# Kernel tuning notes

Measured on AMD Instinct MI355X. Metric: run time of the kernel, lower is better.

## Reference

```python
import jax, jax.numpy as jnp
import numpy as np

D_MODEL = 1024
NUM_HEADS = 16
D_K = D_MODEL // NUM_HEADS
B, S = 2, 2048


def setup_inputs() -> dict:
    key = jax.random.key(0)
    ks = jax.random.split(key, 11)
    scale = 1.0 / np.sqrt(D_MODEL)
    inp = {
        "q": jax.random.normal(ks[0], (B, S, D_MODEL), dtype=jnp.float32),
        "k": jax.random.normal(ks[1], (B, S, D_MODEL), dtype=jnp.float32),
        "v": jax.random.normal(ks[2], (B, S, D_MODEL), dtype=jnp.float32),
        "w_q": jax.random.normal(ks[3], (D_MODEL, D_MODEL), dtype=jnp.float32) * scale,
        "b_q": jnp.zeros((D_MODEL,), dtype=jnp.float32),
        "w_k": jax.random.normal(ks[4], (D_MODEL, D_MODEL), dtype=jnp.float32) * scale,
        "b_k": jnp.zeros((D_MODEL,), dtype=jnp.float32),
        "w_v": jax.random.normal(ks[5], (D_MODEL, D_MODEL), dtype=jnp.float32) * scale,
        "b_v": jnp.zeros((D_MODEL,), dtype=jnp.float32),
        "w_o": jax.random.normal(ks[6], (D_MODEL, D_MODEL), dtype=jnp.float32) * scale,
        "b_o": jnp.zeros((D_MODEL,), dtype=jnp.float32),
    }
    return inp


def reference(q, k, v, w_q, b_q, w_k, b_k, w_v, b_v, w_o, b_o):
    # Linear projections (torch Linear: x @ W^T + b)
    def proj(x, w, b):
        # [B,S,D] -> [B,H,S,d_k]
        y = x @ w.T + b
        return y.reshape(B, S, NUM_HEADS, D_K).transpose(0, 2, 1, 3)

    query = proj(q, w_q, b_q)
    key_ = proj(k, w_k, b_k)
    value = proj(v, w_v, b_v)

    # scores: [B,H,S,S]
    scores = jnp.einsum('bhqd,bhkd->bhqk', query, key_) / jnp.sqrt(
        jnp.asarray(D_K, dtype=query.dtype))
    attn = jax.nn.softmax(scores, axis=-1)
    x = jnp.einsum('bhqk,bhkd->bhqd', attn, value)
    x = x.transpose(0, 2, 1, 3).reshape(B, S, D_MODEL)
    return x @ w_o.T + b_o
```

## Files before the change

### kernel.cpp

```cpp
#include <hip/hip_runtime.h>
#include <stdint.h>

#define D_MODEL 1024
#define NHEAD 16
#define DK 64
#define BATCH 2
#define SEQ 2048
#define MROWS (BATCH * SEQ)
#define KVB 64
#define NIT (SEQ / KVB)
#define QSCALE 0.18033688011112042f

typedef __attribute__((ext_vector_type(8))) __bf16 bf16x8;
typedef __attribute__((ext_vector_type(2))) __bf16 bf16x2;
typedef __attribute__((ext_vector_type(4))) float f32x4;
typedef __attribute__((ext_vector_type(4))) unsigned int u32x4;
typedef __attribute__((ext_vector_type(2))) unsigned int u32x2;

#if defined(__has_builtin)
#if __has_builtin(__builtin_amdgcn_permlane32_swap) && \
    __has_builtin(__builtin_amdgcn_permlane16_swap)
#define HAVE_PERMLANE_SWAP 1
#endif
#endif
#ifndef HAVE_PERMLANE_SWAP
#define HAVE_PERMLANE_SWAP 0
#endif

__device__ __forceinline__ float exp2_hw(float x) {
  return __builtin_amdgcn_exp2f(x);
}

__device__ __forceinline__ f32x4 f4zero() {
  f32x4 z = {0.f, 0.f, 0.f, 0.f};
  return z;
}

__device__ __forceinline__ f32x4 mfma_bf16(bf16x8 a, bf16x8 b, f32x4 c) {
  return __builtin_amdgcn_mfma_f32_16x16x32_bf16(a, b, c, 0, 0, 0);
}

__device__ __forceinline__ void gload_lds16(const void* g, void* l) {
  __builtin_amdgcn_global_load_lds(
      (const __attribute__((address_space(1))) unsigned int*)g,
      (__attribute__((address_space(3))) unsigned int*)l, 16, 0, 0);
}

__device__ __forceinline__ unsigned short f2b(float x) {
  unsigned int u = __float_as_uint(x);
  u += 0x7fffu + ((u >> 16) & 1u);
  return (unsigned short)(u >> 16);
}

#if HAVE_PERMLANE_SWAP
__device__ __forceinline__ u32x2 pl32(unsigned int a, unsigned int b) {
  return __builtin_amdgcn_permlane32_swap(a, b, false, false);
}
__device__ __forceinline__ u32x2 pl16(unsigned int a, unsigned int b) {
  return __builtin_amdgcn_permlane16_swap(a, b, false, false);
}
#endif

__global__ void cvt_all_kernel(const float* __restrict__ q, const float* __restrict__ k,
                               const float* __restrict__ v, const float* __restrict__ wq,
                               const float* __restrict__ wk, const float* __restrict__ wv,
                               const float* __restrict__ wo,
                               unsigned short* __restrict__ actout,
                               unsigned short* __restrict__ wout) {
  const size_t SZA = (size_t)MROWS * D_MODEL;
  const size_t SZW = (size_t)D_MODEL * D_MODEL;
  const int bid = blockIdx.x;
  const float* in;
  unsigned short* out;
  int i;
  if (bid < 12288) {
    const int seg = bid >> 12, ib = bid & 4095;
    in = seg == 0 ? q : seg == 1 ? k : v;
    out = actout + (size_t)seg * SZA;
    i = ib * 256 + threadIdx.x;
  } else {
    const int b2 = bid - 12288;
    const int seg = b2 >> 10, ib = b2 & 1023;
    in = seg == 0 ? wq : seg == 1 ? wk : seg == 2 ? wv : wo;
    out = wout + (size_t)seg * SZW;
    i = ib * 256 + threadIdx.x;
  }
  float4 x = ((const float4*)in)[i];
  ushort4 r;
  r.x = f2b(x.x); r.y = f2b(x.y); r.z = f2b(x.z); r.w = f2b(x.w);
  ((ushort4*)out)[i] = r;
}

template <int EPI, int BROW>
__device__ __forceinline__ void gemm_body128(const unsigned short* __restrict__ A,
                                             const unsigned short* __restrict__ B,
                                             const float* __restrict__ bias,
                                             float scale,
                                             unsigned short* __restrict__ outb,
                                             float* __restrict__ outf, int bx,
                                             int M, int N, int K,
                                             unsigned short* sA, unsigned short* sB) {
  const int tid = threadIdx.x;
  const int w = tid >> 6, l = tid & 63;
  const int nTN = N >> 7;
  const int bm = bx / nTN, bn = bx % nTN;
  const int rowBase = bm << 7, colBase = bn << 7;
  const int wm = w >> 1, wn = w & 1;
  const int g = l >> 4, c16 = l & 15;

  f32x4 acc[4][4];
#pragma unroll
  for (int i = 0; i < 4; i++)
#pragma unroll
    for (int j = 0; j < 4; j++) acc[i][j] = f4zero();

  const int rloc = l >> 2;
  const int uch = (l & 3) ^ (rloc & 3);

  for (int kk = 0; kk < K; kk += 32) {
    __syncthreads();
#pragma unroll
    for (int h = 0; h < 2; h++) {
      const int r0 = w * 16 + h * 64;
      gload_lds16(A + (size_t)(rowBase + r0 + rloc) * K + kk + uch * 8,
                  &sA[r0 * 32]);
      gload_lds16(B + (size_t)(colBase + r0 + rloc) * K + kk + uch * 8,
                  &sB[r0 * 32]);
    }
    __syncthreads();

    bf16x8 af[4], bfr[4];
#pragma unroll
    for (int mt = 0; mt < 4; mt++) {
      const int r = wm * 64 + mt * 16 + c16;
      af[mt] = *(const bf16x8*)&sA[r * 32 + (g ^ (r & 3)) * 8];
    }
#pragma unroll
    for (int nt = 0; nt < 4; nt++) {
      const int r = wn * 64 + nt * 16 + c16;
      bfr[nt] = *(const bf16x8*)&sB[r * 32 + (g ^ (r & 3)) * 8];
    }
#pragma unroll
    for (int mt = 0; mt < 4; mt++)
#pragma unroll
      for (int nt = 0; nt < 4; nt++)
        acc[mt][nt] = mfma_bf16(af[mt], bfr[nt], acc[mt][nt]);
  }

#pragma unroll
  for (int mt = 0; mt < 4; mt++) {
    float brow[4];
    if (BROW) {
#pragma unroll
      for (int i = 0; i < 4; i++)
        brow[i] = bias[rowBase + wm * 64 + mt * 16 + g * 4 + i];
    }
#pragma unroll
    for (int nt = 0; nt < 4; nt++) {
      const int col = colBase + wn * 64 + nt * 16 + c16;
      const float bcol = BROW ? 0.f : bias[col];
#pragma unroll
      for (int i = 0; i < 4; i++) {
        const int row = rowBase + wm * 64 + mt * 16 + g * 4 + i;
        const float bv = BROW ? brow[i] : bcol;
        const float v = (acc[mt][nt][i] + bv) * scale;
        if (EPI == 0)
          outb[(size_t)row * N + col] = f2b(v);
        else
          outf[(size_t)row * N + col] = v;
      }
    }
  }
}

__device__ __forceinline__ void gemm_body64(const unsigned short* __restrict__ A,
                                            const unsigned short* __restrict__ B,
                                            const float* __restrict__ bias,
                                            float* __restrict__ outf, int bx,
                                            int M, int N, int K,
                                            unsigned short* sA, unsigned short* sB) {
  const int tid = threadIdx.x;
  const int w = tid >> 6, l = tid & 63;
  const int nTN = N >> 6;
  const int bm = bx / nTN, bn = bx % nTN;
  const int rowBase = bm << 7, colBase = bn << 6;
  const int g = l >> 4, c16 = l & 15;

  f32x4 acc[2][4];
#pragma unroll
  for (int i = 0; i < 2; i++)
#pragma unroll
    for (int j = 0; j < 4; j++) acc[i][j] = f4zero();

  const int rloc = l >> 2;
  const int uch = (l & 3) ^ (rloc & 3);

  for (int kk = 0; kk < K; kk += 32) {
    __syncthreads();
    gload_lds16(A + (size_t)(rowBase + w * 16 + rloc) * K + kk + uch * 8,
                &sA[(w * 16) * 32]);
    gload_lds16(A + (size_t)(rowBase + 64 + w * 16 + rloc) * K + kk + uch * 8,
                &sA[(64 + w * 16) * 32]);
    gload_lds16(B + (size_t)(colBase + w * 16 + rloc) * K + kk + uch * 8,
                &sB[(w * 16) * 32]);
    __syncthreads();

    bf16x8 af[2], bfr[4];
#pragma unroll
    for (int mt = 0; mt < 2; mt++) {
      const int r = w * 32 + mt * 16 + c16;
      af[mt] = *(const bf16x8*)&sA[r * 32 + (g ^ (r & 3)) * 8];
    }
#pragma unroll
    for (int nt = 0; nt < 4; nt++) {
      const int r = nt * 16 + c16;
      bfr[nt] = *(const bf16x8*)&sB[r * 32 + (g ^ (r & 3)) * 8];
    }
#pragma unroll
    for (int mt = 0; mt < 2; mt++)
#pragma unroll
      for (int nt = 0; nt < 4; nt++)
        acc[mt][nt] = mfma_bf16(af[mt], bfr[nt], acc[mt][nt]);
  }

#pragma unroll
  for (int mt = 0; mt < 2; mt++)
#pragma unroll
    for (int nt = 0; nt < 4; nt++) {
      const int col = colBase + nt * 16 + c16;
      const float bv = bias[col];
#pragma unroll
      for (int i = 0; i < 4; i++) {
        const int row = rowBase + w * 32 + mt * 16 + g * 4 + i;
        outf[(size_t)row * N + col] = acc[mt][nt][i] + bv;
      }
    }
}

__global__ __launch_bounds__(256, 2) void gemm_qkv_kernel(
    const unsigned short* __restrict__ Abase, const unsigned short* __restrict__ Wbase,
    const float* __restrict__ bq, const float* __restrict__ bk,
    const float* __restrict__ bv, unsigned short* __restrict__ QKout,
    unsigned short* __restrict__ VTout) {
  __shared__ __attribute__((aligned(16))) unsigned short sA[128 * 32];
  __shared__ __attribute__((aligned(16))) unsigned short sB[128 * 32];
  const int nblk = 256;
  const int gid = blockIdx.x / nblk, bx = blockIdx.x % nblk;
  const size_t SZA = (size_t)MROWS * D_MODEL;
  const size_t SZW = (size_t)D_MODEL * D_MODEL;
  if (gid < 2) {
    const float* bias = gid == 0 ? bq : bk;
    const float scale = gid == 0 ? QSCALE : 1.0f;
    gemm_body128<0, 0>(Abase + (size_t)gid * SZA, Wbase + (size_t)gid * SZW, bias,
                       scale, QKout + (size_t)gid * SZA, nullptr, bx, MROWS,
                       D_MODEL, D_MODEL, sA, sB);
  } else {
    gemm_body128<0, 1>(Wbase + 2 * SZW, Abase + 2 * SZA, bv, 1.0f, VTout, nullptr,
                       bx, D_MODEL, MROWS, D_MODEL, sA, sB);
  }
}

__global__ __launch_bounds__(256, 4) void gemm_out_kernel(
    const unsigned short* __restrict__ A, const unsigned short* __restrict__ B,
    const float* __restrict__ bias, float* __restrict__ out) {
  __shared__ __attribute__((aligned(16))) unsigned short sA[128 * 32];
  __shared__ __attribute__((aligned(16))) unsigned short sB[64 * 32];
  gemm_body64(A, B, bias, out, blockIdx.x, MROWS, D_MODEL, D_MODEL, sA, sB);
}

__global__ __launch_bounds__(256, 2) void attn_kernel(
    const unsigned short* __restrict__ Qh, const unsigned short* __restrict__ Kh,
    const unsigned short* __restrict__ Vt, unsigned short* __restrict__ Xh) {
  __shared__ __attribute__((aligned(16))) unsigned short sK[2][KVB * 64];
  __shared__ __attribute__((aligned(16))) unsigned short sV[2][64 * KVB];

  const int tid = threadIdx.x, w = tid >> 6, l = tid & 63;
  const int fid = blockIdx.x;
  const int L = (fid & 7) * 64 + (fid >> 3);
  const int bh = L >> 4, qx = L & 15;
  const int b = bh >> 4, h = bh & 15;
  const int q0 = qx * 128 + w * 32;
  const int g = l >> 4, c16 = l & 15;

  bf16x8 qf[2][2];
#pragma unroll
  for (int qs = 0; qs < 2; ++qs)
#pragma unroll
    for (int f = 0; f < 2; ++f)
      qf[qs][f] = *(const bf16x8*)&Qh[(size_t)(b * SEQ + q0 + qs * 16 + c16) * D_MODEL +
                                      h * DK + f * 32 + g * 8];

  const u32x4 onesu = {0x3F803F80u, 0x3F803F80u, 0x3F803F80u, 0x3F803F80u};
  const bf16x8 onesf = __builtin_bit_cast(bf16x8, onesu);

  f32x4 acc[2][4], accl[2];
#pragma unroll
  for (int qs = 0; qs < 2; ++qs) {
#pragma unroll
    for (int dt = 0; dt < 4; ++dt) acc[qs][dt] = f4zero();
    accl[qs] = f4zero();
  }

  const int srow = l >> 3, sch = (l & 7) ^ (srow & 7);

  auto STAGE = [&](int pbuf, int kv0) {
#pragma unroll
    for (int hh = 0; hh < 2; ++hh) {
      const int r0 = w * 16 + hh * 8;
      gload_lds16(
          Kh + (size_t)(b * SEQ + kv0 + r0 + srow) * D_MODEL + h * DK + sch * 8,
          &sK[pbuf][r0 * 64]);
      gload_lds16(Vt + (size_t)(h * DK + r0 + srow) * MROWS + b * SEQ + kv0 + sch * 8,
                  &sV[pbuf][r0 * 64]);
    }
  };

  auto STEP = [&](int PB) {
    f32x4 st[2][4];
#pragma unroll
    for (int kt = 0; kt < 4; ++kt) {
      bf16x8 kf[2];
#pragma unroll
      for (int f = 0; f < 2; ++f) {
        const int key = kt * 16 + c16;
        const int ch = (f * 4 + g) ^ (key & 7);
        kf[f] = *(const bf16x8*)&sK[PB][key * 64 + ch * 8];
      }
#pragma unroll
      for (int qs = 0; qs < 2; ++qs) {
        f32x4 s = mfma_bf16(kf[0], qf[qs][0], f4zero());
        st[qs][kt] = mfma_bf16(kf[1], qf[qs][1], s);
      }
    }

    unsigned int Qpk[2][4][2];
#pragma unroll
    for (int qs = 0; qs < 2; ++qs)
#pragma unroll
      for (int kt = 0; kt < 4; ++kt) {
        float pv[4];
#pragma unroll
        for (int i = 0; i < 4; ++i) pv[i] = exp2_hw(st[qs][kt][i]);
#pragma unroll
        for (int hh = 0; hh < 2; ++hh) {
          bf16x2 t2;
          t2.x = (__bf16)pv[hh * 2];
          t2.y = (__bf16)pv[hh * 2 + 1];
          Qpk[qs][kt][hh] = __builtin_bit_cast(unsigned int, t2);
        }
      }

#pragma unroll
    for (int ks = 0; ks < 2; ++ks) {
      bf16x8 pfrag[2];
#pragma unroll
      for (int qs = 0; qs < 2; ++qs) {
        unsigned int pw[4];
#if HAVE_PERMLANE_SWAP
#pragma unroll
        for (int hh = 0; hh < 2; ++hh) {
          u32x2 s1 = pl32(Qpk[qs][2 * ks][hh], Qpk[qs][2 * ks + 1][hh]);
          u32x2 s2 = pl16(s1.x, s1.y);
          pw[hh] = s2.x;
          pw[2 + hh] = s2.y;
        }
#else
#pragma unroll
        for (int hh = 0; hh < 2; ++hh) {
          const unsigned int a = Qpk[qs][2 * ks][hh], bb = Qpk[qs][2 * ks + 1][hh];
          const unsigned int as = __shfl_xor((int)a, 32);
          const unsigned int bs = __shfl_xor((int)bb, 32);
          const unsigned int r0 = (l >= 32) ? bs : a;
          const unsigned int r1 = (l >= 32) ? bb : as;
          const unsigned int t0 = __shfl_xor((int)r0, 16);
          const unsigned int t1 = __shfl_xor((int)r1, 16);
          pw[hh] = (g & 1) ? t1 : r0;
          pw[2 + hh] = (g & 1) ? r1 : t0;
        }
#endif
        u32x4 pv4 = {pw[0], pw[1], pw[2], pw[3]};
        pfrag[qs] = __builtin_bit_cast(bf16x8, pv4);
      }
      accl[0] = mfma_bf16(pfrag[0], onesf, accl[0]);
      accl[1] = mfma_bf16(pfrag[1], onesf, accl[1]);
#pragma unroll
      for (int dt = 0; dt < 4; ++dt) {
        const int d = dt * 16 + c16;
        const int ch = (ks * 4 + g) ^ (d & 7);
        bf16x8 vfrag = *(const bf16x8*)&sV[PB][d * 64 + ch * 8];
        acc[0][dt] = mfma_bf16(pfrag[0], vfrag, acc[0][dt]);
        acc[1][dt] = mfma_bf16(pfrag[1], vfrag, acc[1][dt]);
      }
    }
  };

  STAGE(0, 0);
  __syncthreads();

  for (int it = 0; it < NIT; it += 2) {
    if (it + 1 < NIT) STAGE(1, (it + 1) * KVB);
    STEP(0);
    __syncthreads();
    if (it + 2 < NIT) STAGE(0, (it + 2) * KVB);
    STEP(1);
    __syncthreads();
  }

#pragma unroll
  for (int qs = 0; qs < 2; ++qs) {
    float linv[4];
#pragma unroll
    for (int i = 0; i < 4; ++i) linv[i] = __builtin_amdgcn_rcpf(accl[qs][i]);
#pragma unroll
    for (int dt = 0; dt < 4; ++dt)
#pragma unroll
      for (int i = 0; i < 4; ++i) {
        const int row = b * SEQ + q0 + qs * 16 + g * 4 + i;
        const int col = h * DK + dt * 16 + c16;
        Xh[(size_t)row * D_MODEL + col] = f2b(acc[qs][dt][i] * linv[i]);
      }
  }
}

extern "C" void kernel_launch(void* const* d_in, const int* in_sizes, int n_in,
                              void* d_out, int out_size, void* d_ws, size_t ws_size,
                              hipStream_t stream) {
  (void)in_sizes; (void)n_in; (void)out_size; (void)ws_size;
  const float* q = (const float*)d_in[0];
  const float* k = (const float*)d_in[1];
  const float* v = (const float*)d_in[2];
  const float* w_q = (const float*)d_in[3];
  const float* b_q = (const float*)d_in[4];
  const float* w_k = (const float*)d_in[5];
  const float* b_k = (const float*)d_in[6];
  const float* w_v = (const float*)d_in[7];
  const float* b_v = (const float*)d_in[8];
  const float* w_o = (const float*)d_in[9];
  const float* b_o = (const float*)d_in[10];

  const size_t SZ_ACT = (size_t)MROWS * D_MODEL;
  const size_t SZ_W = (size_t)D_MODEL * D_MODEL;
  char* ws = (char*)d_ws;
  unsigned short* qb = (unsigned short*)(ws);
  unsigned short* Xh = (unsigned short*)(ws);
  unsigned short* Qproj = (unsigned short*)(ws + 6 * SZ_ACT);
  unsigned short* Vt = (unsigned short*)(ws + 10 * SZ_ACT);
  unsigned short* wqb = (unsigned short*)(ws + 12 * SZ_ACT);
  unsigned short* wob = (unsigned short*)(ws + 12 * SZ_ACT + 6 * SZ_W);

  cvt_all_kernel<<<16384, 256, 0, stream>>>(q, k, v, w_q, w_k, w_v, w_o, qb, wqb);

  gemm_qkv_kernel<<<3 * 256, 256, 0, stream>>>(qb, wqb, b_q, b_k, b_v, Qproj, Vt);

  attn_kernel<<<512, 256, 0, stream>>>(Qproj, Qproj + SZ_ACT, Vt, Xh);

  gemm_out_kernel<<<512, 256, 0, stream>>>(Xh, wob, b_o, (float*)d_out);
}
```

Before: 118.6 us.

## Double attention KV tile to 128 keys, add setprio around PV MFMAs

```diff
diff --git a/kernel.cpp b/kernel.cpp
--- a/kernel.cpp
+++ b/kernel.cpp
@@ -7,7 +7,7 @@
 #define BATCH 2
 #define SEQ 2048
 #define MROWS (BATCH * SEQ)
-#define KVB 64
+#define KVB 128
 #define NIT (SEQ / KVB)
 #define QSCALE 0.18033688011112042f
 
@@ -237,7 +237,7 @@
     }
 }
 
-__global__ __launch_bounds__(256, 2) void gemm_qkv_kernel(
+__global__ __launch_bounds__(256, 3) void gemm_qkv_kernel(
     const unsigned short* __restrict__ Abase, const unsigned short* __restrict__ Wbase,
     const float* __restrict__ bq, const float* __restrict__ bk,
     const float* __restrict__ bv, unsigned short* __restrict__ QKout,
@@ -271,8 +271,8 @@
 __global__ __launch_bounds__(256, 2) void attn_kernel(
     const unsigned short* __restrict__ Qh, const unsigned short* __restrict__ Kh,
     const unsigned short* __restrict__ Vt, unsigned short* __restrict__ Xh) {
-  __shared__ __attribute__((aligned(16))) unsigned short sK[2][KVB * 64];
-  __shared__ __attribute__((aligned(16))) unsigned short sV[2][64 * KVB];
+  __shared__ __attribute__((aligned(16))) unsigned short sK[2][2][64 * 64];
+  __shared__ __attribute__((aligned(16))) unsigned short sV[2][2][64 * 64];
 
   const int tid = threadIdx.x, w = tid >> 6, l = tid & 63;
   const int fid = blockIdx.x;
@@ -305,17 +305,21 @@
 
   auto STAGE = [&](int pbuf, int kv0) {
 #pragma unroll
-    for (int hh = 0; hh < 2; ++hh) {
-      const int r0 = w * 16 + hh * 8;
-      gload_lds16(
-          Kh + (size_t)(b * SEQ + kv0 + r0 + srow) * D_MODEL + h * DK + sch * 8,
-          &sK[pbuf][r0 * 64]);
-      gload_lds16(Vt + (size_t)(h * DK + r0 + srow) * MROWS + b * SEQ + kv0 + sch * 8,
-                  &sV[pbuf][r0 * 64]);
-    }
+    for (int half = 0; half < 2; ++half)
+#pragma unroll
+      for (int hh = 0; hh < 2; ++hh) {
+        const int r0 = w * 16 + hh * 8;
+        const int kvh = kv0 + half * 64;
+        gload_lds16(
+            Kh + (size_t)(b * SEQ + kvh + r0 + srow) * D_MODEL + h * DK + sch * 8,
+            &sK[pbuf][half][r0 * 64]);
+        gload_lds16(
+            Vt + (size_t)(h * DK + r0 + srow) * MROWS + b * SEQ + kvh + sch * 8,
+            &sV[pbuf][half][r0 * 64]);
+      }
   };
 
-  auto STEP = [&](int PB) {
+  auto STEPH = [&](const unsigned short* sKp, const unsigned short* sVp) {
     f32x4 st[2][4];
 #pragma unroll
     for (int kt = 0; kt < 4; ++kt) {
@@ -324,7 +328,7 @@
       for (int f = 0; f < 2; ++f) {
         const int key = kt * 16 + c16;
         const int ch = (f * 4 + g) ^ (key & 7);
-        kf[f] = *(const bf16x8*)&sK[PB][key * 64 + ch * 8];
+        kf[f] = *(const bf16x8*)&sKp[key * 64 + ch * 8];
       }
 #pragma unroll
       for (int qs = 0; qs < 2; ++qs) {
@@ -381,16 +385,18 @@
         u32x4 pv4 = {pw[0], pw[1], pw[2], pw[3]};
         pfrag[qs] = __builtin_bit_cast(bf16x8, pv4);
       }
+      __builtin_amdgcn_s_setprio(1);
       accl[0] = mfma_bf16(pfrag[0], onesf, accl[0]);
       accl[1] = mfma_bf16(pfrag[1], onesf, accl[1]);
 #pragma unroll
       for (int dt = 0; dt < 4; ++dt) {
         const int d = dt * 16 + c16;
         const int ch = (ks * 4 + g) ^ (d & 7);
-        bf16x8 vfrag = *(const bf16x8*)&sV[PB][d * 64 + ch * 8];
+        bf16x8 vfrag = *(const bf16x8*)&sVp[d * 64 + ch * 8];
         acc[0][dt] = mfma_bf16(pfrag[0], vfrag, acc[0][dt]);
         acc[1][dt] = mfma_bf16(pfrag[1], vfrag, acc[1][dt]);
       }
+      __builtin_amdgcn_s_setprio(0);
     }
   };
 
@@ -399,10 +405,12 @@
 
   for (int it = 0; it < NIT; it += 2) {
     if (it + 1 < NIT) STAGE(1, (it + 1) * KVB);
-    STEP(0);
+    STEPH(&sK[0][0][0], &sV[0][0][0]);
+    STEPH(&sK[0][1][0], &sV[0][1][0]);
     __syncthreads();
     if (it + 2 < NIT) STAGE(0, (it + 2) * KVB);
-    STEP(1);
+    STEPH(&sK[1][0][0], &sV[1][0][0]);
+    STEPH(&sK[1][1][0], &sV[1][1][0]);
     __syncthreads();
   }
 
```

After: 117.1 us. Within noise of the previous version (-1.2%).

## Split attention KV range in two and add a combine kernel

Applied to the files above, without the earlier changes.

```diff
diff --git a/kernel.cpp b/kernel.cpp
--- a/kernel.cpp
+++ b/kernel.cpp
@@ -8,7 +8,7 @@
 #define SEQ 2048
 #define MROWS (BATCH * SEQ)
 #define KVB 64
-#define NIT (SEQ / KVB)
+#define NITS 16
 #define QSCALE 0.18033688011112042f
 
 typedef __attribute__((ext_vector_type(8))) __bf16 bf16x8;
@@ -50,6 +50,13 @@
   unsigned int u = __float_as_uint(x);
   u += 0x7fffu + ((u >> 16) & 1u);
   return (unsigned short)(u >> 16);
+}
+
+__device__ __forceinline__ unsigned short f2h(float x) {
+  return __builtin_bit_cast(unsigned short, (_Float16)x);
+}
+__device__ __forceinline__ float h2f(unsigned short u) {
+  return (float)__builtin_bit_cast(_Float16, u);
 }
 
 #if HAVE_PERMLANE_SWAP
@@ -237,7 +244,7 @@
     }
 }
 
-__global__ __launch_bounds__(256, 2) void gemm_qkv_kernel(
+__global__ __launch_bounds__(256, 3) void gemm_qkv_kernel(
     const unsigned short* __restrict__ Abase, const unsigned short* __restrict__ Wbase,
     const float* __restrict__ bq, const float* __restrict__ bk,
     const float* __restrict__ bv, unsigned short* __restrict__ QKout,
@@ -268,18 +275,21 @@
   gemm_body64(A, B, bias, out, blockIdx.x, MROWS, D_MODEL, D_MODEL, sA, sB);
 }
 
-__global__ __launch_bounds__(256, 2) void attn_kernel(
+__global__ __launch_bounds__(256, 4) void attn_kernel(
     const unsigned short* __restrict__ Qh, const unsigned short* __restrict__ Kh,
-    const unsigned short* __restrict__ Vt, unsigned short* __restrict__ Xh) {
+    const unsigned short* __restrict__ Vt, unsigned short* __restrict__ Opart,
+    float* __restrict__ denout) {
   __shared__ __attribute__((aligned(16))) unsigned short sK[2][KVB * 64];
   __shared__ __attribute__((aligned(16))) unsigned short sV[2][64 * KVB];
 
   const int tid = threadIdx.x, w = tid >> 6, l = tid & 63;
   const int fid = blockIdx.x;
-  const int L = (fid & 7) * 64 + (fid >> 3);
-  const int bh = L >> 4, qx = L & 15;
+  const int L = (fid & 7) * 128 + (fid >> 3);
+  const int bh = L >> 5, rem = L & 31;
+  const int split = rem >> 4, qx = rem & 15;
   const int b = bh >> 4, h = bh & 15;
   const int q0 = qx * 128 + w * 32;
+  const int kvbase = split * (SEQ / 2);
   const int g = l >> 4, c16 = l & 15;
 
   bf16x8 qf[2][2];
@@ -307,10 +317,11 @@
 #pragma unroll
     for (int hh = 0; hh < 2; ++hh) {
       const int r0 = w * 16 + hh * 8;
-      gload_lds16(
-          Kh + (size_t)(b * SEQ + kv0 + r0 + srow) * D_MODEL + h * DK + sch * 8,
-          &sK[pbuf][r0 * 64]);
-      gload_lds16(Vt + (size_t)(h * DK + r0 + srow) * MROWS + b * SEQ + kv0 + sch * 8,
+      gload_lds16(Kh + (size_t)(b * SEQ + kvbase + kv0 + r0 + srow) * D_MODEL +
+                      h * DK + sch * 8,
+                  &sK[pbuf][r0 * 64]);
+      gload_lds16(Vt + (size_t)(h * DK + r0 + srow) * MROWS + b * SEQ + kvbase +
+                      kv0 + sch * 8,
                   &sV[pbuf][r0 * 64]);
     }
   };
@@ -381,6 +392,7 @@
         u32x4 pv4 = {pw[0], pw[1], pw[2], pw[3]};
         pfrag[qs] = __builtin_bit_cast(bf16x8, pv4);
       }
+      __builtin_amdgcn_s_setprio(1);
       accl[0] = mfma_bf16(pfrag[0], onesf, accl[0]);
       accl[1] = mfma_bf16(pfrag[1], onesf, accl[1]);
 #pragma unroll
@@ -391,21 +403,24 @@
         acc[0][dt] = mfma_bf16(pfrag[0], vfrag, acc[0][dt]);
         acc[1][dt] = mfma_bf16(pfrag[1], vfrag, acc[1][dt]);
       }
+      __builtin_amdgcn_s_setprio(0);
     }
   };
 
   STAGE(0, 0);
   __syncthreads();
 
-  for (int it = 0; it < NIT; it += 2) {
-    if (it + 1 < NIT) STAGE(1, (it + 1) * KVB);
+  for (int it = 0; it < NITS; it += 2) {
+    if (it + 1 < NITS) STAGE(1, (it + 1) * KVB);
     STEP(0);
     __syncthreads();
-    if (it + 2 < NIT) STAGE(0, (it + 2) * KVB);
+    if (it + 2 < NITS) STAGE(0, (it + 2) * KVB);
     STEP(1);
     __syncthreads();
   }
 
+  unsigned short* Op = Opart + (size_t)split * MROWS * D_MODEL;
+  float* dp = denout + (size_t)split * MROWS * NHEAD;
 #pragma unroll
   for (int qs = 0; qs < 2; ++qs) {
     float linv[4];
@@ -417,9 +432,33 @@
       for (int i = 0; i < 4; ++i) {
         const int row = b * SEQ + q0 + qs * 16 + g * 4 + i;
         const int col = h * DK + dt * 16 + c16;
-        Xh[(size_t)row * D_MODEL + col] = f2b(acc[qs][dt][i] * linv[i]);
-      }
-  }
+        Op[(size_t)row * D_MODEL + col] = f2h(acc[qs][dt][i] * linv[i]);
+      }
+    if (c16 == 0) {
+#pragma unroll
+      for (int i = 0; i < 4; ++i)
+        dp[(size_t)(b * SEQ + q0 + qs * 16 + g * 4 + i) * NHEAD + h] = accl[qs][i];
+    }
+  }
+}
+
+__global__ void combine_kernel(const unsigned short* __restrict__ Opart,
+                               const float* __restrict__ den,
+                               unsigned short* __restrict__ Xh) {
+  const int idx = blockIdx.x * 256 + threadIdx.x;
+  const int row = idx >> 8;
+  const int hd = (idx & 255) >> 4;
+  const float d0 = den[(size_t)row * NHEAD + hd];
+  const float d1 = den[(size_t)MROWS * NHEAD + (size_t)row * NHEAD + hd];
+  const float wsum = __builtin_amdgcn_rcpf(d0 + d1);
+  const ushort4 a = ((const ushort4*)Opart)[idx];
+  const ushort4 bq = ((const ushort4*)(Opart + (size_t)MROWS * D_MODEL))[idx];
+  ushort4 r;
+  r.x = f2b((h2f(a.x) * d0 + h2f(bq.x) * d1) * wsum);
+  r.y = f2b((h2f(a.y) * d0 + h2f(bq.y) * d1) * wsum);
+  r.z = f2b((h2f(a.z) * d0 + h2f(bq.z) * d1) * wsum);
+  r.w = f2b((h2f(a.w) * d0 + h2f(bq.w) * d1) * wsum);
+  ((ushort4*)Xh)[idx] = r;
 }
 
 extern "C" void kernel_launch(void* const* d_in, const int* in_sizes, int n_in,
@@ -443,16 +482,20 @@
   char* ws = (char*)d_ws;
   unsigned short* qb = (unsigned short*)(ws);
   unsigned short* Xh = (unsigned short*)(ws);
+  unsigned short* Opart = (unsigned short*)(ws + 2 * SZ_ACT);
   unsigned short* Qproj = (unsigned short*)(ws + 6 * SZ_ACT);
   unsigned short* Vt = (unsigned short*)(ws + 10 * SZ_ACT);
   unsigned short* wqb = (unsigned short*)(ws + 12 * SZ_ACT);
   unsigned short* wob = (unsigned short*)(ws + 12 * SZ_ACT + 6 * SZ_W);
+  float* den = (float*)(ws + 14 * SZ_ACT);
 
   cvt_all_kernel<<<16384, 256, 0, stream>>>(q, k, v, w_q, w_k, w_v, w_o, qb, wqb);
 
   gemm_qkv_kernel<<<3 * 256, 256, 0, stream>>>(qb, wqb, b_q, b_k, b_v, Qproj, Vt);
 
-  attn_kernel<<<512, 256, 0, stream>>>(Qproj, Qproj + SZ_ACT, Vt, Xh);
+  attn_kernel<<<1024, 256, 0, stream>>>(Qproj, Qproj + SZ_ACT, Vt, Opart, den);
+
+  combine_kernel<<<4096, 256, 0, stream>>>(Opart, den, Xh);
 
   gemm_out_kernel<<<512, 256, 0, stream>>>(Xh, wob, b_o, (float*)d_out);
 }
```

Result: slower. 122.3 us (+3.2%).
